# Performance work log

Hardware: AMD Instinct MI355X
Metric: run time of the kernel (lower is better)

## Reference

```python
import jax, jax.numpy as jnp
import numpy as np

N_NODES = 500000
N_EDGES = 5000000


def _sage_conv(x, edge_index, Wl, bl, Wr):
    # PyG SAGEConv (aggr='mean', root_weight=True):
    #   out = lin_l(mean_{j in N(i)} x_j) + lin_r(x_i)
    # edge_index[0] = source, edge_index[1] = target
    src, dst = edge_index[0], edge_index[1]
    n = x.shape[0]
    msg = x[src]  # [E, F] gather
    agg = jax.ops.segment_sum(msg, dst, num_segments=n)  # [N, F]
    deg = jax.ops.segment_sum(jnp.ones((src.shape[0],), x.dtype), dst, num_segments=n)
    agg = agg / jnp.maximum(deg, 1.0)[:, None]  # mean aggregation
    return agg @ Wl.T + bl + x @ Wr.T


def setup_inputs() -> dict:
    key = jax.random.key(0)
    k1, k2, k3, k4, k5, k6 = jax.random.split(key, 6)
    x = jax.random.normal(k1, (N_NODES, 2), dtype=jnp.float32)
    edge_index = jax.random.randint(k2, (2, N_EDGES), 0, N_NODES, dtype=jnp.int64)
    # conv1: SAGEConv(2, 16); conv2: SAGEConv(16, 1)
    s1 = 1.0 / np.sqrt(2.0)
    s2 = 1.0 / np.sqrt(16.0)
    W1l = jax.random.uniform(k3, (16, 2), jnp.float32, -s1, s1)
    W1r = jax.random.uniform(k4, (16, 2), jnp.float32, -s1, s1)
    b1 = jnp.zeros((16,), jnp.float32)
    W2l = jax.random.uniform(k5, (1, 16), jnp.float32, -s2, s2)
    W2r = jax.random.uniform(k6, (1, 16), jnp.float32, -s2, s2)
    b2 = jnp.zeros((1,), jnp.float32)
    return {"x": x, "edge_index": edge_index,
            "W1l": W1l, "b1": b1, "W1r": W1r,
            "W2l": W2l, "b2": b2, "W2r": W2r}


def reference(x, edge_index, W1l, b1, W1r, W2l, b2, W2r):
    h = jax.nn.relu(_sage_conv(x, edge_index, W1l, b1, W1r))  # [N, 16]
    h = _sage_conv(h, edge_index, W2l, b2, W2r)               # [N, 1]
    return jax.nn.sigmoid(h).squeeze(-1)                      # [N]
```

## Files before the change

kernel.cpp:

```cpp
#include <hip/hip_runtime.h>


static constexpr int BLOCK = 256;
static constexpr int PBLOCK = 1024;
static constexpr int PGRID = 256;
static constexpr int BUCKET_BITS = 10;
static constexpr int BUCKET_NODES = 1 << BUCKET_BITS;
static constexpr int CAP = 16384;
static constexpr int CSTRIDE = 16;
static constexpr int MAXCHUNK = 19584;

static constexpr float S1 = 65536.0f;
static constexpr float IS1 = 1.0f / 65536.0f;
static constexpr long long B1 = 8LL * 65536LL;
static constexpr float S2 = 16384.0f;
static constexpr float IS2 = 1.0f / 16384.0f;
static constexpr int   B2 = 128 * 16384;

__global__ __launch_bounds__(512) void k_init(unsigned* __restrict__ cursor, int NB) {
    int b = blockIdx.x * 512 + threadIdx.x;
    if (b < NB) cursor[(size_t)b * CSTRIDE] = (unsigned)b * (unsigned)CAP;
}

__global__ __launch_bounds__(PBLOCK) void k_part(
    const int* __restrict__ src, const int* __restrict__ dst,
    unsigned* __restrict__ cursor, unsigned* __restrict__ entries,
    int E, int NB)
{
    __shared__ unsigned dstc[MAXCHUNK];
    __shared__ unsigned hist[512];
    __shared__ unsigned base[512];
    int chunk = (E + gridDim.x - 1) / gridDim.x;
    int e0 = blockIdx.x * chunk;
    int e1 = min(e0 + chunk, E);
    int n = e1 - e0;

    for (int b = threadIdx.x; b < NB; b += PBLOCK) hist[b] = 0;
    __syncthreads();
    for (int t = threadIdx.x; t < n; t += PBLOCK) {
        unsigned d = (unsigned)dst[e0 + t];
        dstc[t] = d;
        atomicAdd(&hist[d >> BUCKET_BITS], 1u);
    }
    __syncthreads();
    for (int b0 = threadIdx.x; b0 < NB; b0 += PBLOCK) {
        int b = b0 + (int)(blockIdx.x % (unsigned)NB);
        if (b >= NB) b -= NB;
        base[b] = atomicAdd(&cursor[(size_t)b * CSTRIDE], hist[b]);
    }
    __syncthreads();
    for (int b = threadIdx.x; b < NB; b += PBLOCK) hist[b] = 0;
    __syncthreads();
    for (int t = threadIdx.x; t < n; t += PBLOCK) {
        unsigned d = dstc[t];
        unsigned bk = d >> BUCKET_BITS;
        unsigned r = atomicAdd(&hist[bk], 1u);
        unsigned slot = base[bk] + r;
        unsigned lim = (bk + 1u) * (unsigned)CAP;
        if (slot < lim)
            entries[slot] = ((unsigned)src[e0 + t] << BUCKET_BITS) | (d & (BUCKET_NODES - 1));
    }
}

__global__ __launch_bounds__(BLOCK) void k_agg1(
    const unsigned* __restrict__ entries, const unsigned* __restrict__ cursor,
    const float* __restrict__ x,
    const float* __restrict__ W1l, const float* __restrict__ b1,
    const float* __restrict__ W1r, const float* __restrict__ W2l,
    const float* __restrict__ W2r, const float* __restrict__ b2,
    unsigned* __restrict__ sq, float* __restrict__ t0a, float* __restrict__ inva,
    unsigned* __restrict__ dega, int N)
{
    __shared__ unsigned long long qs[BUCKET_NODES];
    int bk = blockIdx.x;
    for (int i = threadIdx.x; i < BUCKET_NODES; i += BLOCK) qs[i] = 0ULL;
    __syncthreads();

    unsigned start = (unsigned)bk * (unsigned)CAP;
    unsigned end = min(cursor[(size_t)bk * CSTRIDE], start + (unsigned)CAP);
    for (unsigned t = start + threadIdx.x; t < end; t += BLOCK) {
        unsigned en = entries[t];
        unsigned s = en >> BUCKET_BITS;
        unsigned dl = en & (BUCKET_NODES - 1);
        float2 xv = *reinterpret_cast<const float2*>(x + 2 * (size_t)s);
        unsigned q0 = (unsigned)__float2int_rn((xv.x + 8.0f) * S1);
        unsigned q1 = (unsigned)__float2int_rn((xv.y + 8.0f) * S1);
        unsigned long long pk = (1ULL << 56) | ((unsigned long long)q0 << 28)
                              | (unsigned long long)q1;
        atomicAdd(&qs[dl], pk);
    }
    __syncthreads();

    int nodebase = bk << BUCKET_BITS;
    for (int il = threadIdx.x; il < BUCKET_NODES; il += BLOCK) {
        int i = nodebase + il;
        if (i >= N) continue;
        unsigned long long v = qs[il];
        int deg = (int)(v >> 56);
        long long q0 = (long long)((v >> 28) & 0xFFFFFFFULL);
        long long q1 = (long long)(v & 0xFFFFFFFULL);
        long long bias = (long long)deg * B1;
        float inv = 1.0f / (float)max(deg, 1);
        float m0 = (float)(q0 - bias) * IS1 * inv;
        float m1 = (float)(q1 - bias) * IS1 * inv;
        float2 xv = *reinterpret_cast<const float2*>(x + 2 * (size_t)i);
        float s = 0.0f, t0 = b2[0];
#pragma unroll
        for (int o = 0; o < 16; ++o) {
            float h = m0 * W1l[2 * o] + m1 * W1l[2 * o + 1] + b1[o]
                    + xv.x * W1r[2 * o] + xv.y * W1r[2 * o + 1];
            h = fmaxf(h, 0.0f);
            s  += h * W2l[o];
            t0 += h * W2r[o];
        }
        sq[i]   = (unsigned)__float2int_rn((s + 128.0f) * S2);
        t0a[i]  = t0;
        inva[i] = inv;
        dega[i] = (unsigned)deg;
    }
}

__global__ __launch_bounds__(BLOCK) void k_agg2(
    const unsigned* __restrict__ entries, const unsigned* __restrict__ cursor,
    const unsigned* __restrict__ sq,
    const float* __restrict__ t0a, const float* __restrict__ inva,
    const unsigned* __restrict__ dega,
    float* __restrict__ out, int N)
{
    __shared__ unsigned sbin[BUCKET_NODES];
    int bk = blockIdx.x;
    for (int i = threadIdx.x; i < BUCKET_NODES; i += BLOCK) sbin[i] = 0;
    __syncthreads();

    unsigned start = (unsigned)bk * (unsigned)CAP;
    unsigned end = min(cursor[(size_t)bk * CSTRIDE], start + (unsigned)CAP);
    for (unsigned t = start + threadIdx.x; t < end; t += BLOCK) {
        unsigned en = entries[t];
        unsigned s = en >> BUCKET_BITS;
        unsigned dl = en & (BUCKET_NODES - 1);
        atomicAdd(&sbin[dl], sq[s]);
    }
    __syncthreads();

    int nodebase = bk << BUCKET_BITS;
    for (int il = threadIdx.x; il < BUCKET_NODES; il += BLOCK) {
        int i = nodebase + il;
        if (i >= N) continue;
        int deg = (int)dega[i];
        float mean_s = (float)((int)sbin[il] - deg * B2) * IS2 * inva[i];
        out[i] = 1.0f / (1.0f + expf(-(mean_s + t0a[i])));
    }
}

__global__ __launch_bounds__(256) void k_scatter1_fb(
    const int* __restrict__ src, const int* __restrict__ dst,
    const float* __restrict__ x, float* __restrict__ agg1, float* __restrict__ deg, int E)
{
    int stride = gridDim.x * blockDim.x;
    for (int e = blockIdx.x * blockDim.x + threadIdx.x; e < E; e += stride) {
        int s = src[e], d = dst[e];
        float2 xv = *reinterpret_cast<const float2*>(x + 2 * (size_t)s);
        unsafeAtomicAdd(&agg1[2 * (size_t)d + 0], xv.x);
        unsafeAtomicAdd(&agg1[2 * (size_t)d + 1], xv.y);
        unsafeAtomicAdd(&deg[d], 1.0f);
    }
}
__global__ __launch_bounds__(256) void k_node1_fb(
    const float* __restrict__ x, const float* __restrict__ agg1, const float* __restrict__ deg,
    const float* __restrict__ W1l, const float* __restrict__ b1,
    const float* __restrict__ W1r, const float* __restrict__ W2l,
    float* __restrict__ sval, int N)
{
    int i = blockIdx.x * blockDim.x + threadIdx.x;
    if (i >= N) return;
    float inv = 1.0f / fmaxf(deg[i], 1.0f);
    float2 a = *reinterpret_cast<const float2*>(agg1 + 2 * (size_t)i);
    float m0 = a.x * inv, m1 = a.y * inv;
    float2 xv = *reinterpret_cast<const float2*>(x + 2 * (size_t)i);
    float s = 0.0f;
#pragma unroll
    for (int o = 0; o < 16; ++o) {
        float h = m0 * W1l[2 * o] + m1 * W1l[2 * o + 1] + b1[o]
                + xv.x * W1r[2 * o] + xv.y * W1r[2 * o + 1];
        s += fmaxf(h, 0.0f) * W2l[o];
    }
    sval[i] = s;
}
__global__ __launch_bounds__(256) void k_scatter2_fb(
    const int* __restrict__ src, const int* __restrict__ dst,
    const float* __restrict__ sval, float* __restrict__ agg_s, int E)
{
    int stride = gridDim.x * blockDim.x;
    for (int e = blockIdx.x * blockDim.x + threadIdx.x; e < E; e += stride)
        unsafeAtomicAdd(&agg_s[dst[e]], sval[src[e]]);
}
__global__ __launch_bounds__(256) void k_node2_fb(
    const float* __restrict__ x, const float* __restrict__ agg1, const float* __restrict__ deg,
    const float* __restrict__ agg_s,
    const float* __restrict__ W1l, const float* __restrict__ b1,
    const float* __restrict__ W1r, const float* __restrict__ W2r, const float* __restrict__ b2,
    float* __restrict__ out, int N)
{
    int i = blockIdx.x * blockDim.x + threadIdx.x;
    if (i >= N) return;
    float inv = 1.0f / fmaxf(deg[i], 1.0f);
    float2 a = *reinterpret_cast<const float2*>(agg1 + 2 * (size_t)i);
    float m0 = a.x * inv, m1 = a.y * inv;
    float2 xv = *reinterpret_cast<const float2*>(x + 2 * (size_t)i);
    float t = agg_s[i] * inv + b2[0];
#pragma unroll
    for (int o = 0; o < 16; ++o) {
        float h = m0 * W1l[2 * o] + m1 * W1l[2 * o + 1] + b1[o]
                + xv.x * W1r[2 * o] + xv.y * W1r[2 * o + 1];
        t += fmaxf(h, 0.0f) * W2r[o];
    }
    out[i] = 1.0f / (1.0f + expf(-t));
}

extern "C" void kernel_launch(void* const* d_in, const int* in_sizes, int n_in,
                              void* d_out, int out_size, void* d_ws, size_t ws_size,
                              hipStream_t stream) {
    const float* x   = (const float*)d_in[0];
    const int*   ei  = (const int*)d_in[1];
    const float* W1l = (const float*)d_in[2];
    const float* b1  = (const float*)d_in[3];
    const float* W1r = (const float*)d_in[4];
    const float* W2l = (const float*)d_in[5];
    const float* b2  = (const float*)d_in[6];
    const float* W2r = (const float*)d_in[7];

    const int N = in_sizes[0] / 2;
    const int E = in_sizes[1] / 2;
    const int* src = ei;
    const int* dst = ei + (size_t)E;
    float* out = (float*)d_out;

    const int NB = (N + BUCKET_NODES - 1) >> BUCKET_BITS;
    const int chunk = (E + PGRID - 1) / PGRID;

    size_t needed = 512 * CSTRIDE * 4 + (size_t)NB * CAP * 4 + 4 * (size_t)N * 4;
    if (NB <= 512 && chunk <= MAXCHUNK && ws_size >= needed) {
        unsigned* cursor  = (unsigned*)d_ws;
        unsigned* entries = cursor + 512 * CSTRIDE;
        unsigned* sq      = entries + (size_t)NB * CAP;
        float*    t0a     = (float*)(sq + N);
        float*    inva    = t0a + N;
        unsigned* dega    = (unsigned*)(inva + N);

        k_init<<<(NB + 511) / 512, 512, 0, stream>>>(cursor, NB);
        k_part<<<PGRID, PBLOCK, 0, stream>>>(src, dst, cursor, entries, E, NB);
        k_agg1<<<NB, BLOCK, 0, stream>>>(entries, cursor, x, W1l, b1, W1r, W2l, W2r, b2,
                                         sq, t0a, inva, dega, N);
        k_agg2<<<NB, BLOCK, 0, stream>>>(entries, cursor, sq, t0a, inva, dega, out, N);
    } else {
        float* agg1  = (float*)d_ws;
        float* deg   = agg1 + 2 * (size_t)N;
        float* agg_s = deg + (size_t)N;
        float* sval  = agg_s + (size_t)N;
        hipMemsetAsync(d_ws, 0, 4 * (size_t)N * sizeof(float), stream);
        const int eblocks = 2048, nblocks = (N + 255) / 256;
        k_scatter1_fb<<<eblocks, 256, 0, stream>>>(src, dst, x, agg1, deg, E);
        k_node1_fb<<<nblocks, 256, 0, stream>>>(x, agg1, deg, W1l, b1, W1r, W2l, sval, N);
        k_scatter2_fb<<<eblocks, 256, 0, stream>>>(src, dst, sval, agg_s, E);
        k_node2_fb<<<nblocks, 256, 0, stream>>>(x, agg1, deg, agg_s, W1l, b1, W1r, W2r, b2, out, N);
    }
}
```

Measured before the change: 112.1 us.

## Locally sort partition chunks in LDS and write buckets with coalesced stores

The partition kernel now builds a block-local counting sort in shared memory, using a prefix scan over bucket histograms. Each wave then copies whole bucket runs to the global entries array contiguously, replacing scattered per-edge global writes. Edge and entry loads are vectorised to int4/uint4, and the aggregation kernels move to 512-thread blocks. This adds scan barriers and rereads src/dst from global instead of caching dst in LDS, and the uint4 loads assume 16-byte-aligned chunk and bucket starts.

```diff
diff --git a/kernel.cpp b/kernel.cpp
--- a/kernel.cpp
+++ b/kernel.cpp
@@ -1,7 +1,7 @@
 #include <hip/hip_runtime.h>
 
 
-static constexpr int BLOCK = 256;
+static constexpr int ABLOCK = 512;
 static constexpr int PBLOCK = 1024;
 static constexpr int PGRID = 256;
 static constexpr int BUCKET_BITS = 10;
@@ -27,42 +27,103 @@
     unsigned* __restrict__ cursor, unsigned* __restrict__ entries,
     int E, int NB)
 {
-    __shared__ unsigned dstc[MAXCHUNK];
+    __shared__ unsigned sorted[MAXCHUNK];
     __shared__ unsigned hist[512];
+    __shared__ unsigned loc[512];
     __shared__ unsigned base[512];
-    int chunk = (E + gridDim.x - 1) / gridDim.x;
-    int e0 = blockIdx.x * chunk;
-    int e1 = min(e0 + chunk, E);
-    int n = e1 - e0;
-
-    for (int b = threadIdx.x; b < NB; b += PBLOCK) hist[b] = 0;
-    __syncthreads();
-    for (int t = threadIdx.x; t < n; t += PBLOCK) {
-        unsigned d = (unsigned)dst[e0 + t];
-        dstc[t] = d;
-        atomicAdd(&hist[d >> BUCKET_BITS], 1u);
-    }
-    __syncthreads();
-    for (int b0 = threadIdx.x; b0 < NB; b0 += PBLOCK) {
-        int b = b0 + (int)(blockIdx.x % (unsigned)NB);
+    const int tid = threadIdx.x;
+    const int chunk = (E + gridDim.x - 1) / gridDim.x;
+    const int e0 = blockIdx.x * chunk;
+    const int e1 = min(e0 + chunk, E);
+    const int n = e1 - e0;
+    const int nv = n >> 2;
+    const int4* dst4 = reinterpret_cast<const int4*>(dst + e0);
+    const int4* src4 = reinterpret_cast<const int4*>(src + e0);
+
+    for (int b = tid; b < 512; b += PBLOCK) hist[b] = 0;
+    __syncthreads();
+
+    for (int t = tid; t < nv; t += PBLOCK) {
+        int4 d = dst4[t];
+        atomicAdd(&hist[(unsigned)d.x >> BUCKET_BITS], 1u);
+        atomicAdd(&hist[(unsigned)d.y >> BUCKET_BITS], 1u);
+        atomicAdd(&hist[(unsigned)d.z >> BUCKET_BITS], 1u);
+        atomicAdd(&hist[(unsigned)d.w >> BUCKET_BITS], 1u);
+    }
+    for (int e = e0 + (nv << 2) + tid; e < e1; e += PBLOCK)
+        atomicAdd(&hist[(unsigned)dst[e] >> BUCKET_BITS], 1u);
+    __syncthreads();
+
+    if (tid < NB) loc[tid] = hist[tid];
+    __syncthreads();
+    for (int off = 1; off < NB; off <<= 1) {
+        unsigned v = 0;
+        if (tid < NB && tid >= off) v = loc[tid - off];
+        __syncthreads();
+        if (tid < NB) loc[tid] += v;
+        __syncthreads();
+    }
+    if (tid < NB) loc[tid] -= hist[tid];
+
+    if (tid < NB) {
+        int b = tid + (int)(blockIdx.x % (unsigned)NB);
         if (b >= NB) b -= NB;
         base[b] = atomicAdd(&cursor[(size_t)b * CSTRIDE], hist[b]);
     }
     __syncthreads();
-    for (int b = threadIdx.x; b < NB; b += PBLOCK) hist[b] = 0;
-    __syncthreads();
-    for (int t = threadIdx.x; t < n; t += PBLOCK) {
-        unsigned d = dstc[t];
+    for (int b = tid; b < 512; b += PBLOCK) hist[b] = 0;
+    __syncthreads();
+
+    for (int t = tid; t < nv; t += PBLOCK) {
+        int4 d = dst4[t];
+        int4 s = src4[t];
+        {
+            unsigned bk = (unsigned)d.x >> BUCKET_BITS;
+            unsigned r = atomicAdd(&hist[bk], 1u);
+            sorted[loc[bk] + r] = ((unsigned)s.x << BUCKET_BITS) | ((unsigned)d.x & (BUCKET_NODES - 1));
+        }
+        {
+            unsigned bk = (unsigned)d.y >> BUCKET_BITS;
+            unsigned r = atomicAdd(&hist[bk], 1u);
+            sorted[loc[bk] + r] = ((unsigned)s.y << BUCKET_BITS) | ((unsigned)d.y & (BUCKET_NODES - 1));
+        }
+        {
+            unsigned bk = (unsigned)d.z >> BUCKET_BITS;
+            unsigned r = atomicAdd(&hist[bk], 1u);
+            sorted[loc[bk] + r] = ((unsigned)s.z << BUCKET_BITS) | ((unsigned)d.z & (BUCKET_NODES - 1));
+        }
+        {
+            unsigned bk = (unsigned)d.w >> BUCKET_BITS;
+            unsigned r = atomicAdd(&hist[bk], 1u);
+            sorted[loc[bk] + r] = ((unsigned)s.w << BUCKET_BITS) | ((unsigned)d.w & (BUCKET_NODES - 1));
+        }
+    }
+    for (int e = e0 + (nv << 2) + tid; e < e1; e += PBLOCK) {
+        unsigned d = (unsigned)dst[e];
         unsigned bk = d >> BUCKET_BITS;
         unsigned r = atomicAdd(&hist[bk], 1u);
-        unsigned slot = base[bk] + r;
-        unsigned lim = (bk + 1u) * (unsigned)CAP;
-        if (slot < lim)
-            entries[slot] = ((unsigned)src[e0 + t] << BUCKET_BITS) | (d & (BUCKET_NODES - 1));
-    }
-}
-
-__global__ __launch_bounds__(BLOCK) void k_agg1(
+        sorted[loc[bk] + r] = ((unsigned)src[e] << BUCKET_BITS) | (d & (BUCKET_NODES - 1));
+    }
+    __syncthreads();
+
+    const int wave = tid >> 6, lane = tid & 63;
+    const int nw = PBLOCK >> 6;
+    const int off = (int)(blockIdx.x % (unsigned)NB);
+    for (int j = wave; j < NB; j += nw) {
+        int b = j + off;
+        if (b >= NB) b -= NB;
+        unsigned cnt = hist[b];
+        if (cnt == 0) continue;
+        unsigned lo = loc[b], ba = base[b];
+        unsigned lim = (unsigned)(b + 1) * (unsigned)CAP;
+        if (ba >= lim) continue;
+        cnt = min(cnt, lim - ba);
+        for (unsigned i = lane; i < cnt; i += 64)
+            entries[ba + i] = sorted[lo + i];
+    }
+}
+
+__global__ __launch_bounds__(ABLOCK) void k_agg1(
     const unsigned* __restrict__ entries, const unsigned* __restrict__ cursor,
     const float* __restrict__ x,
     const float* __restrict__ W1l, const float* __restrict__ b1,
@@ -73,26 +134,36 @@
 {
     __shared__ unsigned long long qs[BUCKET_NODES];
     int bk = blockIdx.x;
-    for (int i = threadIdx.x; i < BUCKET_NODES; i += BLOCK) qs[i] = 0ULL;
+    for (int i = threadIdx.x; i < BUCKET_NODES; i += ABLOCK) qs[i] = 0ULL;
     __syncthreads();
 
     unsigned start = (unsigned)bk * (unsigned)CAP;
     unsigned end = min(cursor[(size_t)bk * CSTRIDE], start + (unsigned)CAP);
-    for (unsigned t = start + threadIdx.x; t < end; t += BLOCK) {
+    unsigned n = end - start;
+    unsigned nv = n >> 2;
+    const uint4* e4 = reinterpret_cast<const uint4*>(entries + start);
+
+    #define PROC1(en) { \
+        unsigned s_ = (en) >> BUCKET_BITS; \
+        unsigned dl_ = (en) & (BUCKET_NODES - 1); \
+        float2 xv_ = *reinterpret_cast<const float2*>(x + 2 * (size_t)s_); \
+        unsigned q0_ = (unsigned)__float2int_rn((xv_.x + 8.0f) * S1); \
+        unsigned q1_ = (unsigned)__float2int_rn((xv_.y + 8.0f) * S1); \
+        atomicAdd(&qs[dl_], (1ULL << 56) | ((unsigned long long)q0_ << 28) | (unsigned long long)q1_); }
+
+    for (unsigned t = threadIdx.x; t < nv; t += ABLOCK) {
+        uint4 en = e4[t];
+        PROC1(en.x) PROC1(en.y) PROC1(en.z) PROC1(en.w)
+    }
+    for (unsigned t = start + (nv << 2) + threadIdx.x; t < end; t += ABLOCK) {
         unsigned en = entries[t];
-        unsigned s = en >> BUCKET_BITS;
-        unsigned dl = en & (BUCKET_NODES - 1);
-        float2 xv = *reinterpret_cast<const float2*>(x + 2 * (size_t)s);
-        unsigned q0 = (unsigned)__float2int_rn((xv.x + 8.0f) * S1);
-        unsigned q1 = (unsigned)__float2int_rn((xv.y + 8.0f) * S1);
-        unsigned long long pk = (1ULL << 56) | ((unsigned long long)q0 << 28)
-                              | (unsigned long long)q1;
-        atomicAdd(&qs[dl], pk);
-    }
+        PROC1(en)
+    }
+    #undef PROC1
     __syncthreads();
 
     int nodebase = bk << BUCKET_BITS;
-    for (int il = threadIdx.x; il < BUCKET_NODES; il += BLOCK) {
+    for (int il = threadIdx.x; il < BUCKET_NODES; il += ABLOCK) {
         int i = nodebase + il;
         if (i >= N) continue;
         unsigned long long v = qs[il];
@@ -120,7 +191,7 @@
     }
 }
 
-__global__ __launch_bounds__(BLOCK) void k_agg2(
+__global__ __launch_bounds__(ABLOCK) void k_agg2(
     const unsigned* __restrict__ entries, const unsigned* __restrict__ cursor,
     const unsigned* __restrict__ sq,
     const float* __restrict__ t0a, const float* __restrict__ inva,
@@ -129,21 +200,33 @@
 {
     __shared__ unsigned sbin[BUCKET_NODES];
     int bk = blockIdx.x;
-    for (int i = threadIdx.x; i < BUCKET_NODES; i += BLOCK) sbin[i] = 0;
+    for (int i = threadIdx.x; i < BUCKET_NODES; i += ABLOCK) sbin[i] = 0;
     __syncthreads();
 
     unsigned start = (unsigned)bk * (unsigned)CAP;
     unsigned end = min(cursor[(size_t)bk * CSTRIDE], start + (unsigned)CAP);
-    for (unsigned t = start + threadIdx.x; t < end; t += BLOCK) {
+    unsigned n = end - start;
+    unsigned nv = n >> 2;
+    const uint4* e4 = reinterpret_cast<const uint4*>(entries + start);
+
+    #define PROC2(en) { \
+        unsigned s_ = (en) >> BUCKET_BITS; \
+        unsigned dl_ = (en) & (BUCKET_NODES - 1); \
+        atomicAdd(&sbin[dl_], sq[s_]); }
+
+    for (unsigned t = threadIdx.x; t < nv; t += ABLOCK) {
+        uint4 en = e4[t];
+        PROC2(en.x) PROC2(en.y) PROC2(en.z) PROC2(en.w)
+    }
+    for (unsigned t = start + (nv << 2) + threadIdx.x; t < end; t += ABLOCK) {
         unsigned en = entries[t];
-        unsigned s = en >> BUCKET_BITS;
-        unsigned dl = en & (BUCKET_NODES - 1);
-        atomicAdd(&sbin[dl], sq[s]);
-    }
+        PROC2(en)
+    }
+    #undef PROC2
     __syncthreads();
 
     int nodebase = bk << BUCKET_BITS;
-    for (int il = threadIdx.x; il < BUCKET_NODES; il += BLOCK) {
+    for (int il = threadIdx.x; il < BUCKET_NODES; il += ABLOCK) {
         int i = nodebase + il;
         if (i >= N) continue;
         int deg = (int)dega[i];
@@ -249,9 +332,9 @@
 
         k_init<<<(NB + 511) / 512, 512, 0, stream>>>(cursor, NB);
         k_part<<<PGRID, PBLOCK, 0, stream>>>(src, dst, cursor, entries, E, NB);
-        k_agg1<<<NB, BLOCK, 0, stream>>>(entries, cursor, x, W1l, b1, W1r, W2l, W2r, b2,
-                                         sq, t0a, inva, dega, N);
-        k_agg2<<<NB, BLOCK, 0, stream>>>(entries, cursor, sq, t0a, inva, dega, out, N);
+        k_agg1<<<NB, ABLOCK, 0, stream>>>(entries, cursor, x, W1l, b1, W1r, W2l, W2r, b2,
+                                          sq, t0a, inva, dega, N);
+        k_agg2<<<NB, ABLOCK, 0, stream>>>(entries, cursor, sq, t0a, inva, dega, out, N);
     } else {
         float* agg1  = (float*)d_ws;
         float* deg   = agg1 + 2 * (size_t)N;
```

Result: faster. 94.99 us (-15.3%).
